# Performance work log

Hardware: AMD Instinct MI355X
Metric: run time of the kernel (lower is better)

Reference implementation:

```python
import jax, jax.numpy as jnp
import numpy as np

H = 8       # n_heads
E = 128     # embedding_size (= per-head dim)
NEG = -1000000000.0


def setup_inputs() -> dict:
    key = jax.random.key(0)
    ks = jax.random.split(key, 12)
    b, n = 8, 1024
    x = jax.random.normal(ks[0], (b, n, E), dtype=jnp.float32)
    dist = jax.random.normal(ks[1], (b, n, n), dtype=jnp.float32)
    mask = jax.random.randint(ks[2], (b, n), 0, 2).astype(jnp.float32)
    s = 1.0 / np.sqrt(E)
    Wq = jax.random.normal(ks[3], (E, H * E), dtype=jnp.float32) * s
    Wk = jax.random.normal(ks[4], (E, H * E), dtype=jnp.float32) * s
    Wv = jax.random.normal(ks[5], (E, H * E), dtype=jnp.float32) * s
    bq = jnp.zeros((H * E,), jnp.float32)
    bk = jnp.zeros((H * E,), jnp.float32)
    bv = jnp.zeros((H * E,), jnp.float32)
    Wo = jax.random.normal(ks[6], (H * E, E), dtype=jnp.float32) * (1.0 / np.sqrt(H * E))
    bo = jnp.zeros((E,), jnp.float32)
    return {"x": x, "dist": dist, "mask": mask, "Wq": Wq, "bq": bq,
            "Wk": Wk, "bk": bk, "Wv": Wv, "bv": bv, "Wo": Wo, "bo": bo}


def reference(x, dist, mask, Wq, bq, Wk, bk, Wv, bv, Wo, bo):
    b, n, e = x.shape
    scale = e ** (-0.5)
    # project and split heads: [b, n, H*E] -> [b, H, n, E]
    def heads(W, bias):
        return (x @ W + bias).reshape(b, n, H, e).transpose(0, 2, 1, 3)
    q = heads(Wq, bq) * mask[:, None, :, None]
    k = heads(Wk, bk) * mask[:, None, :, None]
    v = heads(Wv, bv) * mask[:, None, :, None]
    # scores with additive distance bias broadcast over heads
    a = jnp.einsum('bhqe,bhke->bhqk', q * scale, k) + dist[:, None, :, :]
    am = jnp.einsum('bq,bk->bqk', mask, mask)[:, None, :, :]  # [b,1,n,n]
    a = jnp.where(am == 0, NEG, a)
    a = jax.nn.softmax(a, axis=-1)
    a = jnp.where(am == 0, 0.0, a)
    y = jnp.einsum('bhqk,bhke->bhqe', a, v)
    y = y.transpose(0, 2, 1, 3).reshape(b, n, H * e)
    y = y @ Wo + bo
    return y * mask[:, :, None]
```

## Files before the change

### kernel.cpp

```cpp
#include <hip/hip_runtime.h>
#include <hip/hip_bf16.h>

#define NH 8
#define ED 128
#define NB 8
#define NN 1024

typedef __attribute__((ext_vector_type(8))) short s16x8;
typedef __attribute__((ext_vector_type(8))) __bf16 bf16x8_t;
typedef __attribute__((ext_vector_type(4))) float f32x4;
typedef __attribute__((ext_vector_type(16))) float f32x16;
typedef __attribute__((ext_vector_type(4))) unsigned int u32x4;

static __device__ __forceinline__ unsigned short f2bf(float f) {
    union { float f; unsigned u; } v; v.f = f;
    unsigned r = v.u + 0x7fffu + ((v.u >> 16) & 1u);
    return (unsigned short)(r >> 16);
}

static __device__ __forceinline__ f32x4 mfma16(s16x8 a, s16x8 b, f32x4 c) {
    return __builtin_amdgcn_mfma_f32_16x16x32_bf16(
        __builtin_bit_cast(bf16x8_t, a), __builtin_bit_cast(bf16x8_t, b), c, 0, 0, 0);
}

static __device__ __forceinline__ f32x16 mfma32(s16x8 a, s16x8 b, f32x16 c) {
    return __builtin_amdgcn_mfma_f32_32x32x16_bf16(
        __builtin_bit_cast(bf16x8_t, a), __builtin_bit_cast(bf16x8_t, b), c, 0, 0, 0);
}

static __device__ __forceinline__ unsigned cvtpk(float lo, float hi) {
    unsigned r;
    asm("v_cvt_pk_bf16_f32 %0, %1, %2" : "=v"(r) : "v"(lo), "v"(hi));
    return r;
}

__global__ __launch_bounds__(256) void prep_kernel(
    const float* __restrict__ x,
    const float* __restrict__ Wq, const float* __restrict__ Wk,
    const float* __restrict__ Wv, const float* __restrict__ Wo,
    unsigned short* __restrict__ xb,
    unsigned short* __restrict__ wqt, unsigned short* __restrict__ wkt,
    unsigned short* __restrict__ wvt, unsigned short* __restrict__ wot) {
    int bid = blockIdx.x, tid = threadIdx.x;
    if (bid < 1024) {
        int i = bid * 256 + tid;
        float4 v = ((const float4*)x)[i];
        unsigned long long pk = (unsigned long long)f2bf(v.x)
                              | ((unsigned long long)f2bf(v.y) << 16)
                              | ((unsigned long long)f2bf(v.z) << 32)
                              | ((unsigned long long)f2bf(v.w) << 48);
        ((unsigned long long*)xb)[i] = pk;
        return;
    }
    const float* in; unsigned short* outp; int rows_in, cols_in, i;
    if (bid < 1536)      { in = Wq; outp = wqt; rows_in = 128;  cols_in = 1024; i = (bid - 1024) * 256 + tid; }
    else if (bid < 2048) { in = Wk; outp = wkt; rows_in = 128;  cols_in = 1024; i = (bid - 1536) * 256 + tid; }
    else if (bid < 2560) { in = Wv; outp = wvt; rows_in = 128;  cols_in = 1024; i = (bid - 2048) * 256 + tid; }
    else                 { in = Wo; outp = wot; rows_in = 1024; cols_in = 128;  i = (bid - 2560) * 256 + tid; }
    int c = i / rows_in;
    int r = i - c * rows_in;
    outp[i] = f2bf(in[(size_t)r * cols_in + c]);
}

__global__ __launch_bounds__(256) void qkv_kernel(
    const unsigned short* __restrict__ xb,
    const unsigned short* __restrict__ wqt,
    const unsigned short* __restrict__ wkt,
    const unsigned short* __restrict__ wvt,
    const float* __restrict__ bq, const float* __restrict__ bk, const float* __restrict__ bv,
    unsigned short* __restrict__ q_ws,
    unsigned short* __restrict__ k_ws,
    unsigned short* __restrict__ v_ws) {
    int bid = blockIdx.x;
    int mt = bid / 24, c = bid % 24;
    int which = c >> 3;
    int c0 = (c & 7) * 128;
    int m0 = mt * 128;
    int tid = threadIdx.x;
    int w = tid >> 6, lane = tid & 63, g = lane >> 4, r15 = lane & 15;
    int wr = (w >> 1) * 64, wc = (w & 1) * 64;

    const unsigned short* wt = (which == 0) ? wqt : (which == 1) ? wkt : wvt;
    const float* bias = (which == 0) ? bq : (which == 1) ? bk : bv;

    const f32x4 fzero = {0.f, 0.f, 0.f, 0.f};
    f32x4 acc[4][4];
#pragma unroll
    for (int i = 0; i < 4; i++)
#pragma unroll
        for (int j = 0; j < 4; j++) acc[i][j] = fzero;

#pragma unroll
    for (int kf = 0; kf < 4; kf++) {
        s16x8 af[4], bfr[4];
#pragma unroll
        for (int mf = 0; mf < 4; mf++)
            af[mf] = *(const s16x8*)(xb + (size_t)(m0 + wr + mf * 16 + r15) * ED + kf * 32 + g * 8);
#pragma unroll
        for (int nf = 0; nf < 4; nf++)
            bfr[nf] = *(const s16x8*)(wt + (size_t)(c0 + wc + nf * 16 + r15) * ED + kf * 32 + g * 8);
#pragma unroll
        for (int mf = 0; mf < 4; mf++)
#pragma unroll
            for (int nf = 0; nf < 4; nf++)
                acc[mf][nf] = mfma16(af[mf], bfr[nf], acc[mf][nf]);
    }

    float scale = (which == 0) ? 0.08838834764831845f : 1.0f;

#pragma unroll
    for (int nf = 0; nf < 4; nf++) {
        int col = c0 + wc + nf * 16 + r15;
        float bv_ = bias[col];
        int hh = col >> 7, e = col & 127;
#pragma unroll
        for (int mf = 0; mf < 4; mf++) {
#pragma unroll
            for (int rr = 0; rr < 4; rr++) {
                int row = m0 + wr + mf * 16 + g * 4 + rr;
                int bb = row >> 10, n = row & 1023;
                float val = (acc[mf][nf][rr] + bv_) * scale;
                if (which == 2)
                    v_ws[((size_t)(bb * NH + hh) * ED + e) * NN + n] = f2bf(val);
                else if (which == 0)
                    q_ws[((size_t)(bb * NH + hh) * NN + n) * ED + e] = f2bf(val);
                else
                    k_ws[((size_t)(bb * NH + hh) * NN + n) * ED + e] = f2bf(val);
            }
        }
    }
}

__global__ __launch_bounds__(512) void attn_kernel(
    const unsigned short* __restrict__ q_ws,
    const unsigned short* __restrict__ k_ws,
    const unsigned short* __restrict__ v_ws,
    const float* __restrict__ dist,
    const float* __restrict__ mask,
    unsigned short* __restrict__ y_ws) {
    int p = blockIdx.x;
    int b = p & 7, j = p >> 3;
    int head = j >> 2, qt = j & 3;
    int bh = b * NH + head;
    int q0 = qt * 256;

    int tid = threadIdx.x;
    int w = tid >> 6, lane = tid & 63;
    int e31 = lane & 31, h = lane >> 5;
    bool h0 = (h == 0);

    __shared__ __align__(16) unsigned short Kl[8192];
    __shared__ __align__(16) unsigned short Vl[8192];
    __shared__ __align__(16) float mk_s[NN];

    const unsigned short* kbase = k_ws + (size_t)bh * NN * ED;
    const unsigned short* vbase = v_ws + (size_t)bh * ED * NN;

    mk_s[tid] = mask[b * NN + tid];
    mk_s[tid + 512] = mask[b * NN + tid + 512];

    int qrow = q0 + w * 32 + e31;
    const float* drow = dist + ((size_t)b * NN + qrow) * NN;

    s16x8 qf[8];
    const unsigned short* qb = q_ws + ((size_t)bh * NN + qrow) * ED + h * 8;
#pragma unroll
    for (int es = 0; es < 8; ++es) qf[es] = *(const s16x8*)(qb + es * 16);

    const f32x16 fz16 = {0.f,0.f,0.f,0.f,0.f,0.f,0.f,0.f,0.f,0.f,0.f,0.f,0.f,0.f,0.f,0.f};
    f32x16 o0 = fz16, o1 = fz16, o2 = fz16, o3 = fz16;
    float l_r = 0.f;

    int k_key = tid >> 3, k_e8 = tid & 7;
    const unsigned short* kgsrc = kbase + k_key * ED + k_e8 * 8;
    int k_wb0 = ((k_e8 * 2 + (k_key >> 5)) * 32 + (k_key & 31)) * 16;
    int k_wb1 = (((k_e8 + 8) * 2 + (k_key >> 5)) * 32 + (k_key & 31)) * 16;
    int v_e = tid >> 2, v_k8 = tid & 3;
    const unsigned short* vgsrc = vbase + (size_t)v_e * NN + v_k8 * 8;
    int v_wb0 = (v_k8 * 128 + v_e) * 16;
    int v_wb1 = ((v_k8 + 4) * 128 + v_e) * 16;

    const char* Kp = (const char*)Kl + h * 1024 + e31 * 16;
    const char* Vp = (const char*)Vl + h * 2048 + e31 * 16;

    s16x8 kreg0 = *(const s16x8*)(kgsrc);
    s16x8 kreg1 = *(const s16x8*)(kgsrc + 64);
    s16x8 vreg0 = *(const s16x8*)(vgsrc);
    s16x8 vreg1 = *(const s16x8*)(vgsrc + 32);

    for (int kt = 0; kt < 16; ++kt) {
        int k0 = kt * 64;
        *(s16x8*)((char*)Kl + k_wb0) = kreg0;
        *(s16x8*)((char*)Kl + k_wb1) = kreg1;
        *(s16x8*)((char*)Vl + v_wb0) = vreg0;
        *(s16x8*)((char*)Vl + v_wb1) = vreg1;
        __syncthreads();

        if (kt < 15) {
            const unsigned short* kn = kgsrc + (size_t)(kt + 1) * 64 * ED;
            kreg0 = *(const s16x8*)(kn);
            kreg1 = *(const s16x8*)(kn + 64);
            const unsigned short* vn = vgsrc + k0 + 64;
            vreg0 = *(const s16x8*)(vn);
            vreg1 = *(const s16x8*)(vn + 32);
        }

        f32x16 sA0 = fz16, sA1 = fz16;
#pragma unroll
        for (int es = 0; es < 8; ++es) {
            s16x8 kb0 = *(const s16x8*)(Kp + es * 2048);
            s16x8 kb1 = *(const s16x8*)(Kp + es * 2048 + 512);
            sA0 = mfma32(kb0, qf[es], sA0);
            sA1 = mfma32(kb1, qf[es], sA1);
        }

        float pp[32];
#pragma unroll
        for (int kf = 0; kf < 2; ++kf) {
#pragma unroll
            for (int rc = 0; rc < 4; ++rc) {
                int cb = k0 + kf * 32 + rc * 8 + 4 * h;
                f32x4 d4 = *(const f32x4*)(drow + cb);
                f32x4 m4 = *(const f32x4*)(&mk_s[cb]);
#pragma unroll
                for (int jj = 0; jj < 4; ++jj) {
                    float sv = kf ? sA1[rc * 4 + jj] : sA0[rc * 4 + jj];
                    float pv = __expf(sv + d4[jj] - 16.0f) * m4[jj];
                    pp[kf * 16 + rc * 4 + jj] = pv;
                    l_r += pv;
                }
            }
        }

#pragma unroll
        for (int kf = 0; kf < 2; ++kf) {
#pragma unroll
            for (int ks2 = 0; ks2 < 2; ++ks2) {
                const float* pb = &pp[kf * 16 + ks2 * 8];
                unsigned X0 = cvtpk(pb[0], pb[1]);
                unsigned X1 = cvtpk(pb[2], pb[3]);
                unsigned Y0 = cvtpk(pb[4], pb[5]);
                unsigned Y1 = cvtpk(pb[6], pb[7]);
                unsigned sx0 = (unsigned)__shfl_xor((int)X0, 32, 64);
                unsigned sx1 = (unsigned)__shfl_xor((int)X1, 32, 64);
                unsigned sy0 = (unsigned)__shfl_xor((int)Y0, 32, 64);
                unsigned sy1 = (unsigned)__shfl_xor((int)Y1, 32, 64);
                u32x4 pw;
                pw[0] = h0 ? X0 : sy0;
                pw[1] = h0 ? X1 : sy1;
                pw[2] = h0 ? sx0 : Y0;
                pw[3] = h0 ? sx1 : Y1;
                s16x8 pa = __builtin_bit_cast(s16x8, pw);
                int kstep = kf * 2 + ks2;
                const char* vp = Vp + kstep * 4096;
                o0 = mfma32(pa, *(const s16x8*)(vp), o0);
                o1 = mfma32(pa, *(const s16x8*)(vp + 512), o1);
                o2 = mfma32(pa, *(const s16x8*)(vp + 1024), o2);
                o3 = mfma32(pa, *(const s16x8*)(vp + 1536), o3);
            }
        }
        __syncthreads();
    }

    float lt = l_r + __shfl_xor(l_r, 32, 64);
    float inv = (lt > 0.f) ? 1.0f / lt : 0.f;
#pragma unroll
    for (int rc = 0; rc < 4; ++rc) {
#pragma unroll
        for (int jj = 0; jj < 4; ++jj) {
            int qq = jj + 8 * rc + 4 * h;
            float iq = __shfl(inv, qq, 64);
            int row = q0 + w * 32 + qq;
            size_t base = ((size_t)b * NN + row) * (NH * ED) + head * ED + e31;
            y_ws[base]      = f2bf(o0[rc * 4 + jj] * iq);
            y_ws[base + 32] = f2bf(o1[rc * 4 + jj] * iq);
            y_ws[base + 64] = f2bf(o2[rc * 4 + jj] * iq);
            y_ws[base + 96] = f2bf(o3[rc * 4 + jj] * iq);
        }
    }
}

__global__ __launch_bounds__(256) void oproj_kernel(
    const unsigned short* __restrict__ y_ws,
    const unsigned short* __restrict__ wot,
    const float* __restrict__ bo,
    const float* __restrict__ mask,
    float* __restrict__ outp) {
    int bid = blockIdx.x;
    int mt = bid >> 1, nt = bid & 1;
    int m0 = mt * 64, c0 = nt * 64;
    int tid = threadIdx.x;
    int w = tid >> 6, lane = tid & 63, g = lane >> 4, r15 = lane & 15;

    const f32x4 fzero = {0.f, 0.f, 0.f, 0.f};
    f32x4 acc[4];
#pragma unroll
    for (int i = 0; i < 4; i++) acc[i] = fzero;

    const unsigned short* arow = y_ws + (size_t)(m0 + w * 16 + r15) * (NH * ED);
    for (int kt = 0; kt < 32; ++kt) {
        s16x8 af = *(const s16x8*)(arow + kt * 32 + g * 8);
#pragma unroll
        for (int nf = 0; nf < 4; nf++) {
            s16x8 bfr = *(const s16x8*)(wot + (size_t)(c0 + nf * 16 + r15) * (NH * ED) + kt * 32 + g * 8);
            acc[nf] = mfma16(af, bfr, acc[nf]);
        }
    }
#pragma unroll
    for (int nf = 0; nf < 4; nf++) {
        int col = c0 + nf * 16 + r15;
        float bias = bo[col];
#pragma unroll
        for (int rr = 0; rr < 4; rr++) {
            int token = m0 + w * 16 + g * 4 + rr;
            outp[(size_t)token * ED + col] = (acc[nf][rr] + bias) * mask[token];
        }
    }
}

extern "C" void kernel_launch(void* const* d_in, const int* in_sizes, int n_in,
                              void* d_out, int out_size, void* d_ws, size_t ws_size,
                              hipStream_t stream) {
    const float* x    = (const float*)d_in[0];
    const float* dist = (const float*)d_in[1];
    const float* mask = (const float*)d_in[2];
    const float* Wq   = (const float*)d_in[3];
    const float* bq   = (const float*)d_in[4];
    const float* Wk   = (const float*)d_in[5];
    const float* bk   = (const float*)d_in[6];
    const float* Wv   = (const float*)d_in[7];
    const float* bv   = (const float*)d_in[8];
    const float* Wo   = (const float*)d_in[9];
    const float* bo   = (const float*)d_in[10];
    float* outp = (float*)d_out;

    char* ws = (char*)d_ws;
    unsigned short* xb   = (unsigned short*)(ws);
    unsigned short* wqt  = (unsigned short*)(ws + (2u << 20));
    unsigned short* wkt  = (unsigned short*)(ws + (2u << 20) + (256u << 10));
    unsigned short* wvt  = (unsigned short*)(ws + (2u << 20) + (512u << 10));
    unsigned short* wot  = (unsigned short*)(ws + (2u << 20) + (768u << 10));
    unsigned short* q_ws = (unsigned short*)(ws + (3u << 20));
    unsigned short* k_ws = (unsigned short*)(ws + (19u << 20));
    unsigned short* v_ws = (unsigned short*)(ws + (35u << 20));
    unsigned short* y_ws = (unsigned short*)(ws + (51u << 20));

    prep_kernel<<<3072, 256, 0, stream>>>(x, Wq, Wk, Wv, Wo, xb, wqt, wkt, wvt, wot);
    qkv_kernel<<<1536, 256, 0, stream>>>(xb, wqt, wkt, wvt, bq, bk, bv, q_ws, k_ws, v_ws);
    attn_kernel<<<256, 512, 0, stream>>>(q_ws, k_ws, v_ws, dist, mask, y_ws);
    oproj_kernel<<<256, 256, 0, stream>>>(y_ws, wot, bo, mask, outp);
}
```

Baseline: 153.6 us.

## Pre-swizzle K/V tiles, fp16 dist with mask, async LDS double-buffer in attention

A new prep kernel converts dist to fp16, folds the key mask into it as a large negative value, and lays it out in the per-thread order the attention kernel reads. The QKV kernel now writes K and V already tiled in the LDS layout. This lets the attention kernel fill double-buffered LDS with global_load_lds directly, with no register staging. The attention grid changes from 256 blocks of 512 threads to 512 blocks of 256 threads over 128-row query tiles. The aim is to halve dist traffic inside attention and overlap K/V loads with compute. The cost is an extra full pass over dist, fp16 rounding of dist, and the mask now entering only through exp of a large negative value.

```diff
diff --git a/kernel.cpp b/kernel.cpp
--- a/kernel.cpp
+++ b/kernel.cpp
@@ -1,5 +1,6 @@
 #include <hip/hip_runtime.h>
 #include <hip/hip_bf16.h>
+#include <hip/hip_fp16.h>
 
 #define NH 8
 #define ED 128
@@ -32,6 +33,11 @@
     unsigned r;
     asm("v_cvt_pk_bf16_f32 %0, %1, %2" : "=v"(r) : "v"(lo), "v"(hi));
     return r;
+}
+
+static __device__ __forceinline__ void gll16(const void* g, void* l) {
+    __builtin_amdgcn_global_load_lds((const __attribute__((address_space(1))) void*)g,
+                                     (__attribute__((address_space(3))) void*)l, 16, 0, 0);
 }
 
 __global__ __launch_bounds__(256) void prep_kernel(
@@ -62,6 +68,44 @@
     outp[i] = f2bf(in[(size_t)r * cols_in + c]);
 }
 
+__global__ __launch_bounds__(256) void prep_dist_kernel(
+    const float* __restrict__ dist,
+    const float* __restrict__ mask,
+    unsigned short* __restrict__ dswz) {
+    int bid = blockIdx.x;
+    int c = bid & 3;
+    int t = bid >> 2;
+    int kt = t & 15; t >>= 4;
+    int qt = t & 7;
+    int b = t >> 3;
+    int tid = threadIdx.x;
+    int h = (tid >> 5) & 1;
+    int row = qt * 128 + (tid >> 6) * 32 + (tid & 31);
+    int colbase = kt * 64 + (c >> 1) * 32 + (c & 1) * 16 + 4 * h;
+
+    const float* dr = dist + ((size_t)b * NN + row) * NN;
+    const float* mr = mask + (size_t)b * NN;
+    f32x4 dA = *(const f32x4*)(dr + colbase);
+    f32x4 dB = *(const f32x4*)(dr + colbase + 8);
+    f32x4 mA = *(const f32x4*)(mr + colbase);
+    f32x4 mB = *(const f32x4*)(mr + colbase + 8);
+
+    unsigned short o[8];
+#pragma unroll
+    for (int jj = 0; jj < 4; ++jj) {
+        o[jj]     = (mA[jj] == 0.0f) ? (unsigned short)0xFBFF
+                                     : __half_as_ushort(__float2half_rn(dA[jj]));
+        o[4 + jj] = (mB[jj] == 0.0f) ? (unsigned short)0xFBFF
+                                     : __half_as_ushort(__float2half_rn(dB[jj]));
+    }
+    u32x4 pk;
+    pk[0] = (unsigned)o[0] | ((unsigned)o[1] << 16);
+    pk[1] = (unsigned)o[2] | ((unsigned)o[3] << 16);
+    pk[2] = (unsigned)o[4] | ((unsigned)o[5] << 16);
+    pk[3] = (unsigned)o[6] | ((unsigned)o[7] << 16);
+    *(u32x4*)(dswz + ((size_t)bid * 256 + tid) * 8) = pk;
+}
+
 __global__ __launch_bounds__(256) void qkv_kernel(
     const unsigned short* __restrict__ xb,
     const unsigned short* __restrict__ wqt,
@@ -119,49 +163,49 @@
             for (int rr = 0; rr < 4; rr++) {
                 int row = m0 + wr + mf * 16 + g * 4 + rr;
                 int bb = row >> 10, n = row & 1023;
+                int bh = bb * NH + hh;
                 float val = (acc[mf][nf][rr] + bv_) * scale;
-                if (which == 2)
-                    v_ws[((size_t)(bb * NH + hh) * ED + e) * NN + n] = f2bf(val);
-                else if (which == 0)
-                    q_ws[((size_t)(bb * NH + hh) * NN + n) * ED + e] = f2bf(val);
-                else
-                    k_ws[((size_t)(bb * NH + hh) * NN + n) * ED + e] = f2bf(val);
+                if (which == 0) {
+                    q_ws[((size_t)bh * NN + n) * ED + e] = f2bf(val);
+                } else if (which == 1) {
+                    int ktl = n >> 6, k = n & 63;
+                    int slot = (e >> 4) * 128 + ((e >> 3) & 1) * 64 + (k >> 5) * 32 + (k & 31);
+                    k_ws[(size_t)(bh * 16 + ktl) * 8192 + slot * 8 + (e & 7)] = f2bf(val);
+                } else {
+                    int ktl = n >> 6, k = n & 63;
+                    int slot = (k >> 4) * 256 + ((k >> 3) & 1) * 128 + (e >> 5) * 32 + (e & 31);
+                    v_ws[(size_t)(bh * 16 + ktl) * 8192 + slot * 8 + (k & 7)] = f2bf(val);
+                }
             }
         }
     }
 }
 
-__global__ __launch_bounds__(512) void attn_kernel(
+__global__ __launch_bounds__(256) void attn_kernel(
     const unsigned short* __restrict__ q_ws,
     const unsigned short* __restrict__ k_ws,
     const unsigned short* __restrict__ v_ws,
-    const float* __restrict__ dist,
-    const float* __restrict__ mask,
+    const unsigned short* __restrict__ dswz,
     unsigned short* __restrict__ y_ws) {
     int p = blockIdx.x;
-    int b = p & 7, j = p >> 3;
-    int head = j >> 2, qt = j & 3;
+    int b = p & 7, r = p >> 3;
+    int head = r >> 3, qt = r & 7;
     int bh = b * NH + head;
-    int q0 = qt * 256;
+    int q0 = qt * 128;
 
     int tid = threadIdx.x;
     int w = tid >> 6, lane = tid & 63;
     int e31 = lane & 31, h = lane >> 5;
     bool h0 = (h == 0);
 
-    __shared__ __align__(16) unsigned short Kl[8192];
-    __shared__ __align__(16) unsigned short Vl[8192];
-    __shared__ __align__(16) float mk_s[NN];
-
-    const unsigned short* kbase = k_ws + (size_t)bh * NN * ED;
-    const unsigned short* vbase = v_ws + (size_t)bh * ED * NN;
-
-    mk_s[tid] = mask[b * NN + tid];
-    mk_s[tid + 512] = mask[b * NN + tid + 512];
+    __shared__ __align__(16) unsigned short Kl[2][8192];
+    __shared__ __align__(16) unsigned short Vl[2][8192];
+
+    const char* kg = (const char*)k_ws + (size_t)bh * 16 * 16384;
+    const char* vg = (const char*)v_ws + (size_t)bh * 16 * 16384;
+    const char* dq = (const char*)dswz + ((size_t)(b * 8 + qt) << 18);
 
     int qrow = q0 + w * 32 + e31;
-    const float* drow = dist + ((size_t)b * NN + qrow) * NN;
-
     s16x8 qf[8];
     const unsigned short* qb = q_ws + ((size_t)bh * NN + qrow) * ED + h * 8;
 #pragma unroll
@@ -171,40 +215,33 @@
     f32x16 o0 = fz16, o1 = fz16, o2 = fz16, o3 = fz16;
     float l_r = 0.f;
 
-    int k_key = tid >> 3, k_e8 = tid & 7;
-    const unsigned short* kgsrc = kbase + k_key * ED + k_e8 * 8;
-    int k_wb0 = ((k_e8 * 2 + (k_key >> 5)) * 32 + (k_key & 31)) * 16;
-    int k_wb1 = (((k_e8 + 8) * 2 + (k_key >> 5)) * 32 + (k_key & 31)) * 16;
-    int v_e = tid >> 2, v_k8 = tid & 3;
-    const unsigned short* vgsrc = vbase + (size_t)v_e * NN + v_k8 * 8;
-    int v_wb0 = (v_k8 * 128 + v_e) * 16;
-    int v_wb1 = ((v_k8 + 4) * 128 + v_e) * 16;
-
-    const char* Kp = (const char*)Kl + h * 1024 + e31 * 16;
-    const char* Vp = (const char*)Vl + h * 2048 + e31 * 16;
-
-    s16x8 kreg0 = *(const s16x8*)(kgsrc);
-    s16x8 kreg1 = *(const s16x8*)(kgsrc + 64);
-    s16x8 vreg0 = *(const s16x8*)(vgsrc);
-    s16x8 vreg1 = *(const s16x8*)(vgsrc + 32);
+#pragma unroll
+    for (int pass = 0; pass < 4; ++pass) {
+        gll16(kg + (pass * 256 + tid) * 16, (char*)&Kl[0][0] + pass * 4096 + w * 1024);
+        gll16(vg + (pass * 256 + tid) * 16, (char*)&Vl[0][0] + pass * 4096 + w * 1024);
+    }
+    __syncthreads();
 
     for (int kt = 0; kt < 16; ++kt) {
-        int k0 = kt * 64;
-        *(s16x8*)((char*)Kl + k_wb0) = kreg0;
-        *(s16x8*)((char*)Kl + k_wb1) = kreg1;
-        *(s16x8*)((char*)Vl + v_wb0) = vreg0;
-        *(s16x8*)((char*)Vl + v_wb1) = vreg1;
-        __syncthreads();
-
+        int cur = kt & 1;
         if (kt < 15) {
-            const unsigned short* kn = kgsrc + (size_t)(kt + 1) * 64 * ED;
-            kreg0 = *(const s16x8*)(kn);
-            kreg1 = *(const s16x8*)(kn + 64);
-            const unsigned short* vn = vgsrc + k0 + 64;
-            vreg0 = *(const s16x8*)(vn);
-            vreg1 = *(const s16x8*)(vn + 32);
-        }
-
+            const char* kn = kg + (size_t)(kt + 1) * 16384;
+            const char* vn = vg + (size_t)(kt + 1) * 16384;
+            char* kd = (char*)&Kl[cur ^ 1][0] + w * 1024;
+            char* vd = (char*)&Vl[cur ^ 1][0] + w * 1024;
+#pragma unroll
+            for (int pass = 0; pass < 4; ++pass) {
+                gll16(kn + (pass * 256 + tid) * 16, kd + pass * 4096);
+                gll16(vn + (pass * 256 + tid) * 16, vd + pass * 4096);
+            }
+        }
+
+        u32x4 dch[4];
+#pragma unroll
+        for (int c = 0; c < 4; ++c)
+            dch[c] = *(const u32x4*)(dq + ((size_t)(kt * 4 + c) * 256 + tid) * 16);
+
+        const char* Kp = (const char*)&Kl[cur][0] + h * 1024 + e31 * 16;
         f32x16 sA0 = fz16, sA1 = fz16;
 #pragma unroll
         for (int es = 0; es < 8; ++es) {
@@ -216,22 +253,21 @@
 
         float pp[32];
 #pragma unroll
-        for (int kf = 0; kf < 2; ++kf) {
-#pragma unroll
-            for (int rc = 0; rc < 4; ++rc) {
-                int cb = k0 + kf * 32 + rc * 8 + 4 * h;
-                f32x4 d4 = *(const f32x4*)(drow + cb);
-                f32x4 m4 = *(const f32x4*)(&mk_s[cb]);
-#pragma unroll
-                for (int jj = 0; jj < 4; ++jj) {
-                    float sv = kf ? sA1[rc * 4 + jj] : sA0[rc * 4 + jj];
-                    float pv = __expf(sv + d4[jj] - 16.0f) * m4[jj];
-                    pp[kf * 16 + rc * 4 + jj] = pv;
-                    l_r += pv;
-                }
+        for (int c = 0; c < 4; ++c) {
+#pragma unroll
+            for (int u = 0; u < 8; ++u) {
+                int i = c * 8 + u;
+                unsigned wv = dch[c][u >> 1];
+                float dv = __half2float(__ushort_as_half(
+                    (unsigned short)((u & 1) ? (wv >> 16) : (wv & 0xffff))));
+                float sv = (i < 16) ? sA0[i] : sA1[i - 16];
+                float pv = __expf(sv + dv - 16.0f);
+                pp[i] = pv;
+                l_r += pv;
             }
         }
 
+        const char* Vp = (const char*)&Vl[cur][0] + h * 2048 + e31 * 16;
 #pragma unroll
         for (int kf = 0; kf < 2; ++kf) {
 #pragma unroll
@@ -344,9 +380,11 @@
     unsigned short* k_ws = (unsigned short*)(ws + (19u << 20));
     unsigned short* v_ws = (unsigned short*)(ws + (35u << 20));
     unsigned short* y_ws = (unsigned short*)(ws + (51u << 20));
+    unsigned short* dswz = (unsigned short*)(ws + (67u << 20));
 
     prep_kernel<<<3072, 256, 0, stream>>>(x, Wq, Wk, Wv, Wo, xb, wqt, wkt, wvt, wot);
+    prep_dist_kernel<<<4096, 256, 0, stream>>>(dist, mask, dswz);
     qkv_kernel<<<1536, 256, 0, stream>>>(xb, wqt, wkt, wvt, bq, bk, bv, q_ws, k_ws, v_ws);
-    attn_kernel<<<256, 512, 0, stream>>>(q_ws, k_ws, v_ws, dist, mask, y_ws);
+    attn_kernel<<<512, 256, 0, stream>>>(q_ws, k_ws, v_ws, dswz, y_ws);
     oproj_kernel<<<256, 256, 0, stream>>>(y_ws, wot, bo, mask, outp);
 }
```

After: 136.0 us. 1.13x faster.
